# Kernel optimization log

Measured on AMD Instinct MI355X. Metric: run time of the kernel, lower is better.

The kernel has to match this reference:

```python
import jax, jax.numpy as jnp
import numpy as np

BATCH = 8192
FEATS = 4096
RATE = 0.1
ANNEAL = 0.5 + 0.1  # self.anneal = 0.5 + anneal


def setup_inputs() -> dict:
    key = jax.random.key(0)
    k1, k2 = jax.random.split(key)
    inputs = jax.random.normal(k1, (BATCH, FEATS), dtype=jnp.float32)
    # standard-normal draws, one per feature (replaces the serial map_fn RNG)
    noise = jax.random.normal(k2, (FEATS,), dtype=jnp.float32)
    return {"inputs": inputs, "noise": noise}


def reference(inputs, noise):
    # SegDropout (training path), agg_method='mean', noise_type='gaussian'
    F = inputs.shape[-1]
    x_agg = jnp.mean(inputs, axis=0)                      # [F] batch-wise aggregate
    x_min = jnp.min(x_agg)
    x_max = jnp.max(x_agg)
    # quantize each feature's aggregate into one of F+1 integer bins
    bins = (F * (x_agg - x_min) / (x_max - x_min)).astype(jnp.int32)  # [F], values in [0, F]
    # unique_with_counts + gather(counts, idx) == histogram lookup per feature
    counts_per_bin = jnp.bincount(bins, length=F + 1)      # [F+1]
    counts = counts_per_bin[bins].astype(inputs.dtype)     # [F] count of each feature's bin
    dr = RATE ** (1.0 / (ANNEAL * counts))                 # annealed per-bin dropout rate
    dr = jnp.where(counts == 1.0, jnp.asarray(RATE, inputs.dtype), dr)
    sigma = jnp.sqrt(dr / (1.0 - dr))                      # [F]
    # multiplicative Gaussian noise ~ N(1, sigma) per feature
    return inputs * (1.0 + sigma * noise)
```

## Files before the change

kernel.cpp:

```cpp
#include <hip/hip_runtime.h>

#define BATCH 8192
#define FEATS 4096
#define CHUNKS 128
#define ROWS_PER_CHUNK (BATCH / CHUNKS)


__global__ __launch_bounds__(256) void colsum_part(const float* __restrict__ in,
                                                   double* __restrict__ partials) {
    const int colBase = blockIdx.x * 1024 + threadIdx.x * 4;
    const int row0 = blockIdx.y * ROWS_PER_CHUNK;
    const float4* p = (const float4*)in + (size_t)row0 * (FEATS / 4) + (colBase >> 2);
    double a0 = 0.0, a1 = 0.0, a2 = 0.0, a3 = 0.0;
#pragma unroll 8
    for (int r = 0; r < ROWS_PER_CHUNK; ++r) {
        float4 v = p[(size_t)r * (FEATS / 4)];
        a0 += (double)v.x; a1 += (double)v.y; a2 += (double)v.z; a3 += (double)v.w;
    }
    double* dst = partials + (size_t)blockIdx.y * FEATS + colBase;
    dst[0] = a0; dst[1] = a1; dst[2] = a2; dst[3] = a3;
}

__global__ __launch_bounds__(256) void reduce_mean(const double* __restrict__ partials,
                                                   double* __restrict__ means) {
    const int c = blockIdx.x * 256 + threadIdx.x;
    double s = 0.0;
#pragma unroll 8
    for (int k = 0; k < CHUNKS; ++k) s += partials[(size_t)k * FEATS + c];
    means[c] = s * (1.0 / (double)BATCH);
}

__global__ __launch_bounds__(1024) void config_kernel(const double* __restrict__ means,
                                                      const float* __restrict__ noise,
                                                      float* __restrict__ scale) {
    __shared__ double s_mean[FEATS];
    __shared__ double s_red[1024];
    __shared__ unsigned s_hist[FEATS + 1];
    const int tid = threadIdx.x;

    double lmin = 1e300, lmax = -1e300;
#pragma unroll
    for (int k = 0; k < 4; ++k) {
        int c = tid + k * 1024;
        double m = means[c];
        s_mean[c] = m;
        lmin = fmin(lmin, m);
        lmax = fmax(lmax, m);
    }
    s_red[tid] = lmin; __syncthreads();
    for (int s = 512; s > 0; s >>= 1) {
        if (tid < s) s_red[tid] = fmin(s_red[tid], s_red[tid + s]);
        __syncthreads();
    }
    const double xmin = s_red[0]; __syncthreads();
    s_red[tid] = lmax; __syncthreads();
    for (int s = 512; s > 0; s >>= 1) {
        if (tid < s) s_red[tid] = fmax(s_red[tid], s_red[tid + s]);
        __syncthreads();
    }
    const double xmax = s_red[0]; __syncthreads();

    for (int i = tid; i < FEATS + 1; i += 1024) s_hist[i] = 0;
    __syncthreads();

    int binr[4];
    const double denom = xmax - xmin;
#pragma unroll
    for (int k = 0; k < 4; ++k) {
        int c = tid + k * 1024;
        double b = ((double)FEATS * (s_mean[c] - xmin)) / denom;
        int bi = (int)b;
        binr[k] = bi;
        atomicAdd(&s_hist[bi], 1u);
    }
    __syncthreads();

    const double K = -2.302585092994045684017991454684364208;
#pragma unroll
    for (int k = 0; k < 4; ++k) {
        int c = tid + k * 1024;
        unsigned cnt = s_hist[binr[k]];
        double dr = (cnt == 1u) ? 0.1 : exp(K / (0.6 * (double)cnt));
        double sg = sqrt(dr / (1.0 - dr));
        scale[c] = (float)(1.0 + sg * (double)noise[c]);
    }
}

__global__ __launch_bounds__(256) void scale_kernel(const float4* __restrict__ in,
                                                    const float4* __restrict__ scale,
                                                    float4* __restrict__ out) {
    const int i = blockIdx.x * 256 + threadIdx.x;
    float4 v = in[i];
    float4 s = scale[i & (FEATS / 4 - 1)];
    v.x *= s.x; v.y *= s.y; v.z *= s.z; v.w *= s.w;
    out[i] = v;
}

extern "C" void kernel_launch(void* const* d_in, const int* in_sizes, int n_in,
                              void* d_out, int out_size, void* d_ws, size_t ws_size,
                              hipStream_t stream) {
    const float* in = (const float*)d_in[0];
    const float* noise = (const float*)d_in[1];
    float* out = (float*)d_out;
    double* partials = (double*)d_ws;
    double* means = partials + (size_t)CHUNKS * FEATS;
    float* scale = (float*)(means + FEATS);

    dim3 g1(4, CHUNKS);
    colsum_part<<<g1, 256, 0, stream>>>(in, partials);
    reduce_mean<<<FEATS / 256, 256, 0, stream>>>(partials, means);
    config_kernel<<<1, 1024, 0, stream>>>(means, noise, scale);
    scale_kernel<<<BATCH * FEATS / 4 / 256, 256, 0, stream>>>(
        (const float4*)in, (const float4*)scale, (float4*)out);
}
```

Before: 260.0 us.

## Split colsum finer, fold min/max into reduce, per-bin sigma, nontemporal scale stores

Doubles the row chunks in the column-sum pass to launch more blocks. Moves the min/max reduction into reduce_mean as per-block partials, and config_kernel now computes sigma once per histogram bin instead of once per feature. The scale kernel handles four float4s per thread and writes the output with nontemporal stores to reduce cache pollution. The cost is a larger partials buffer and a second read of the means from global memory in the single-block config kernel.

```diff
diff --git a/kernel.cpp b/kernel.cpp
--- a/kernel.cpp
+++ b/kernel.cpp
@@ -2,19 +2,21 @@
 
 #define BATCH 8192
 #define FEATS 4096
-#define CHUNKS 128
-#define ROWS_PER_CHUNK (BATCH / CHUNKS)
+#define RCHUNKS 256
+#define ROWS_PER_CHUNK (BATCH / RCHUNKS)
+
+typedef float v4f __attribute__((ext_vector_type(4)));
 
 
 __global__ __launch_bounds__(256) void colsum_part(const float* __restrict__ in,
                                                    double* __restrict__ partials) {
     const int colBase = blockIdx.x * 1024 + threadIdx.x * 4;
     const int row0 = blockIdx.y * ROWS_PER_CHUNK;
-    const float4* p = (const float4*)in + (size_t)row0 * (FEATS / 4) + (colBase >> 2);
+    const v4f* p = (const v4f*)in + (size_t)row0 * (FEATS / 4) + (colBase >> 2);
     double a0 = 0.0, a1 = 0.0, a2 = 0.0, a3 = 0.0;
 #pragma unroll 8
     for (int r = 0; r < ROWS_PER_CHUNK; ++r) {
-        float4 v = p[(size_t)r * (FEATS / 4)];
+        v4f v = p[(size_t)r * (FEATS / 4)];
         a0 += (double)v.x; a1 += (double)v.y; a2 += (double)v.z; a3 += (double)v.w;
     }
     double* dst = partials + (size_t)blockIdx.y * FEATS + colBase;
@@ -22,78 +24,89 @@
 }
 
 __global__ __launch_bounds__(256) void reduce_mean(const double* __restrict__ partials,
-                                                   double* __restrict__ means) {
-    const int c = blockIdx.x * 256 + threadIdx.x;
+                                                   double* __restrict__ means,
+                                                   double* __restrict__ bmin,
+                                                   double* __restrict__ bmax) {
+    const int tid = threadIdx.x;
+    const int c = blockIdx.x * 256 + tid;
     double s = 0.0;
 #pragma unroll 8
-    for (int k = 0; k < CHUNKS; ++k) s += partials[(size_t)k * FEATS + c];
-    means[c] = s * (1.0 / (double)BATCH);
+    for (int k = 0; k < RCHUNKS; ++k) s += partials[(size_t)k * FEATS + c];
+    const double m = s * (1.0 / (double)BATCH);
+    means[c] = m;
+    __shared__ double smin[256], smax[256];
+    smin[tid] = m; smax[tid] = m; __syncthreads();
+    for (int s2 = 128; s2 > 0; s2 >>= 1) {
+        if (tid < s2) {
+            smin[tid] = fmin(smin[tid], smin[tid + s2]);
+            smax[tid] = fmax(smax[tid], smax[tid + s2]);
+        }
+        __syncthreads();
+    }
+    if (tid == 0) { bmin[blockIdx.x] = smin[0]; bmax[blockIdx.x] = smax[0]; }
 }
 
 __global__ __launch_bounds__(1024) void config_kernel(const double* __restrict__ means,
+                                                      const double* __restrict__ bmin,
+                                                      const double* __restrict__ bmax,
                                                       const float* __restrict__ noise,
                                                       float* __restrict__ scale) {
-    __shared__ double s_mean[FEATS];
-    __shared__ double s_red[1024];
     __shared__ unsigned s_hist[FEATS + 1];
+    __shared__ double s_sig[FEATS + 1];
     const int tid = threadIdx.x;
 
-    double lmin = 1e300, lmax = -1e300;
+    double xmin = bmin[0], xmax = bmax[0];
 #pragma unroll
-    for (int k = 0; k < 4; ++k) {
-        int c = tid + k * 1024;
-        double m = means[c];
-        s_mean[c] = m;
-        lmin = fmin(lmin, m);
-        lmax = fmax(lmax, m);
+    for (int i = 1; i < FEATS / 256; ++i) {
+        xmin = fmin(xmin, bmin[i]);
+        xmax = fmax(xmax, bmax[i]);
     }
-    s_red[tid] = lmin; __syncthreads();
-    for (int s = 512; s > 0; s >>= 1) {
-        if (tid < s) s_red[tid] = fmin(s_red[tid], s_red[tid + s]);
-        __syncthreads();
-    }
-    const double xmin = s_red[0]; __syncthreads();
-    s_red[tid] = lmax; __syncthreads();
-    for (int s = 512; s > 0; s >>= 1) {
-        if (tid < s) s_red[tid] = fmax(s_red[tid], s_red[tid + s]);
-        __syncthreads();
-    }
-    const double xmax = s_red[0]; __syncthreads();
-
     for (int i = tid; i < FEATS + 1; i += 1024) s_hist[i] = 0;
     __syncthreads();
 
     int binr[4];
+    double nz[4];
     const double denom = xmax - xmin;
 #pragma unroll
     for (int k = 0; k < 4; ++k) {
         int c = tid + k * 1024;
-        double b = ((double)FEATS * (s_mean[c] - xmin)) / denom;
+        double b = ((double)FEATS * (means[c] - xmin)) / denom;
         int bi = (int)b;
         binr[k] = bi;
+        nz[k] = (double)noise[c];
         atomicAdd(&s_hist[bi], 1u);
     }
     __syncthreads();
 
     const double K = -2.302585092994045684017991454684364208;
+    for (int i = tid; i < FEATS + 1; i += 1024) {
+        unsigned cnt = s_hist[i];
+        if (cnt) {
+            double dr = (cnt == 1u) ? 0.1 : exp(K / (0.6 * (double)cnt));
+            s_sig[i] = sqrt(dr / (1.0 - dr));
+        }
+    }
+    __syncthreads();
+
 #pragma unroll
     for (int k = 0; k < 4; ++k) {
         int c = tid + k * 1024;
-        unsigned cnt = s_hist[binr[k]];
-        double dr = (cnt == 1u) ? 0.1 : exp(K / (0.6 * (double)cnt));
-        double sg = sqrt(dr / (1.0 - dr));
-        scale[c] = (float)(1.0 + sg * (double)noise[c]);
+        scale[c] = (float)(1.0 + s_sig[binr[k]] * nz[k]);
     }
 }
 
-__global__ __launch_bounds__(256) void scale_kernel(const float4* __restrict__ in,
-                                                    const float4* __restrict__ scale,
-                                                    float4* __restrict__ out) {
-    const int i = blockIdx.x * 256 + threadIdx.x;
-    float4 v = in[i];
-    float4 s = scale[i & (FEATS / 4 - 1)];
-    v.x *= s.x; v.y *= s.y; v.z *= s.z; v.w *= s.w;
-    out[i] = v;
+__global__ __launch_bounds__(256) void scale_kernel(const v4f* __restrict__ in,
+                                                    const v4f* __restrict__ scalev,
+                                                    v4f* __restrict__ out) {
+    const int base = blockIdx.x * 1024 + threadIdx.x;
+#pragma unroll
+    for (int k = 0; k < 4; ++k) {
+        const int i = base + k * 256;
+        v4f v = in[i];
+        v4f s = scalev[i & (FEATS / 4 - 1)];
+        v *= s;
+        __builtin_nontemporal_store(v, &out[i]);
+    }
 }
 
 extern "C" void kernel_launch(void* const* d_in, const int* in_sizes, int n_in,
@@ -103,13 +116,15 @@
     const float* noise = (const float*)d_in[1];
     float* out = (float*)d_out;
     double* partials = (double*)d_ws;
-    double* means = partials + (size_t)CHUNKS * FEATS;
-    float* scale = (float*)(means + FEATS);
+    double* means = partials + (size_t)RCHUNKS * FEATS;
+    double* bmin = means + FEATS;
+    double* bmax = bmin + 16;
+    float* scale = (float*)(bmax + 16);
 
-    dim3 g1(4, CHUNKS);
+    dim3 g1(4, RCHUNKS);
     colsum_part<<<g1, 256, 0, stream>>>(in, partials);
-    reduce_mean<<<FEATS / 256, 256, 0, stream>>>(partials, means);
-    config_kernel<<<1, 1024, 0, stream>>>(means, noise, scale);
-    scale_kernel<<<BATCH * FEATS / 4 / 256, 256, 0, stream>>>(
-        (const float4*)in, (const float4*)scale, (float4*)out);
+    reduce_mean<<<FEATS / 256, 256, 0, stream>>>(partials, means, bmin, bmax);
+    config_kernel<<<1, 1024, 0, stream>>>(means, bmin, bmax, noise, scale);
+    scale_kernel<<<BATCH * FEATS / 4 / 1024, 256, 0, stream>>>(
+        (const v4f*)in, (const v4f*)scale, (v4f*)out);
 }
```

Measured after the change: 268.9 us. 3.4% more time.
